# Optimization experiments

Measured on AMD Instinct MI355X. Metric: run time of the kernel, lower is better.

The kernel has to match this reference:

```python
import jax, jax.numpy as jnp
import numpy as np

LAG = 168
HORIZON = 24
D = 6            # d_model = 1 feature + 5-dim position embedding
FF = 18          # dim_feedforward
NL = 3           # num encoder layers
B = 8192
EPS = 1e-5


def setup_inputs() -> dict:
    key = jax.random.key(0)
    ks = jax.random.split(key, 16)
    s = 0.1
    return {
        "input": jax.random.normal(ks[0], (B, LAG), dtype=jnp.float32),
        "pos_emb": jax.random.normal(ks[1], (LAG, 5), dtype=jnp.float32) * s,
        "in_proj_w": jax.random.normal(ks[2], (NL, 3 * D, D), dtype=jnp.float32) * s,
        "in_proj_b": jax.random.normal(ks[3], (NL, 3 * D), dtype=jnp.float32) * s,
        "out_w": jax.random.normal(ks[4], (NL, D, D), dtype=jnp.float32) * s,
        "out_b": jax.random.normal(ks[5], (NL, D), dtype=jnp.float32) * s,
        "ln1_g": jnp.ones((NL, D), dtype=jnp.float32),
        "ln1_b": jnp.zeros((NL, D), dtype=jnp.float32),
        "lin1_w": jax.random.normal(ks[6], (NL, FF, D), dtype=jnp.float32) * s,
        "lin1_b": jax.random.normal(ks[7], (NL, FF), dtype=jnp.float32) * s,
        "lin2_w": jax.random.normal(ks[8], (NL, D, FF), dtype=jnp.float32) * s,
        "lin2_b": jax.random.normal(ks[9], (NL, D), dtype=jnp.float32) * s,
        "ln2_g": jnp.ones((NL, D), dtype=jnp.float32),
        "ln2_b": jnp.zeros((NL, D), dtype=jnp.float32),
        "head_w": jax.random.normal(ks[10], (HORIZON, D * LAG), dtype=jnp.float32) * s,
        "head_b": jax.random.normal(ks[11], (HORIZON,), dtype=jnp.float32) * s,
    }


def _layer_norm(x, g, b):
    m = jnp.mean(x, axis=-1, keepdims=True)
    v = jnp.mean((x - m) ** 2, axis=-1, keepdims=True)
    return (x - m) * jax.lax.rsqrt(v + EPS) * g + b


def reference(input, pos_emb, in_proj_w, in_proj_b, out_w, out_b,
              ln1_g, ln1_b, lin1_w, lin1_b, lin2_w, lin2_b,
              ln2_g, ln2_b, head_w, head_b):
    Bsz, L = input.shape
    # embed positions and concat with raw feature -> [B, L, 6]
    x = jnp.concatenate(
        [input[..., None], jnp.broadcast_to(pos_emb[None], (Bsz, L, 5))], axis=2)

    h = x
    scale = 1.0 / jnp.sqrt(jnp.float32(D))
    for i in range(NL):  # post-norm TransformerEncoderLayer (PyTorch default)
        qkv = jnp.einsum("bld,ed->ble", h, in_proj_w[i]) + in_proj_b[i]  # [B,L,18]
        q, k, v = jnp.split(qkv, 3, axis=-1)  # each [B,L,6], single head
        scores = jnp.einsum("bqd,bkd->bqk", q, k) * scale
        attn = jax.nn.softmax(scores, axis=-1)
        o = jnp.einsum("bqk,bkd->bqd", attn, v)
        o = jnp.einsum("bld,ed->ble", o, out_w[i]) + out_b[i]
        h = _layer_norm(h + o, ln1_g[i], ln1_b[i])
        f = jax.nn.relu(jnp.einsum("bld,fd->blf", h, lin1_w[i]) + lin1_b[i])
        f = jnp.einsum("blf,df->bld", f, lin2_w[i]) + lin2_b[i]
        h = _layer_norm(h + f, ln2_g[i], ln2_b[i])

    h = jax.nn.relu(h + x)              # residual from embedded input + relu
    h = h.reshape(Bsz, L * D)           # flatten
    return h @ head_w.T + head_b        # [B, HORIZON]
```

## Files before the change

### kernel.cpp

```cpp
#include <hip/hip_runtime.h>
#include <math.h>

#define LAG 168
#define HOR 24
#define DM 6
#define FFD 18
#define NL 3
#define WPB 4
#define LNEPS 1e-5f

typedef unsigned int u32;
typedef float f32x4 __attribute__((ext_vector_type(4)));
typedef float f32x16 __attribute__((ext_vector_type(16)));
typedef short s16x8 __attribute__((ext_vector_type(8)));
typedef __bf16 bfx2 __attribute__((ext_vector_type(2)));

#define PP    800
#define SLICE 1376

__device__ __forceinline__ u32 pkbf(float a, float b) {
    bfx2 t; t[0] = (__bf16)a; t[1] = (__bf16)b;
    return __builtin_bit_cast(u32, t);
}
__device__ __forceinline__ s16x8 mk8(u32 a, u32 b, u32 c, u32 d) {
    uint4 u; u.x = a; u.y = b; u.z = c; u.w = d;
    return __builtin_bit_cast(s16x8, u);
}
__device__ __forceinline__ float b2f(unsigned short h) {
    u32 u = ((u32)h) << 16; return __builtin_bit_cast(float, u);
}
__device__ __forceinline__ void ln6(const float* r, const float* g, const float* bb, float* outv) {
    float m = (r[0]+r[1]+r[2]+r[3]+r[4]+r[5]) * (1.0f/6.0f);
    float v = 0.f;
#pragma unroll
    for (int d = 0; d < DM; ++d) { float t = r[d]-m; v += t*t; }
    v *= (1.0f/6.0f);
    float rs = __builtin_amdgcn_rsqf(v + LNEPS);
#pragma unroll
    for (int d = 0; d < DM; ++d) outv[d] = (r[d]-m)*rs*g[d] + bb[d];
}

__global__ __launch_bounds__(64*WPB) void tfenc_kernel(
    const float* __restrict__ input, const float* __restrict__ pos_emb,
    const float* __restrict__ ipw, const float* __restrict__ ipb,
    const float* __restrict__ ow,  const float* __restrict__ obp,
    const float* __restrict__ l1g, const float* __restrict__ l1b,
    const float* __restrict__ f1w, const float* __restrict__ f1b,
    const float* __restrict__ f2w, const float* __restrict__ f2b,
    const float* __restrict__ l2g, const float* __restrict__ l2b,
    const float* __restrict__ hw,  const float* __restrict__ hb,
    float* __restrict__ out)
{
    __shared__ __align__(16) float lds[WPB * SLICE];

    const int L   = threadIdx.x & 63;
    const int wid = threadIdx.x >> 6;
    const int b   = blockIdx.x * WPB + wid;

    float*  sl  = lds + wid * SLICE;
    __bf16* slh = (__bf16*)sl;
    u32*    slu = (u32*)sl;

    float hv[3][DM], xv[3][DM];
#pragma unroll
    for (int i = 0; i < 3; ++i) {
        int r = L + 64*i;
        bool real = (r < LAG);
        xv[i][0] = real ? input[(size_t)b*LAG + r] : 0.f;
#pragma unroll
        for (int j = 0; j < 5; ++j)
            xv[i][1+j] = real ? pos_emb[r*5 + j] : 0.f;
#pragma unroll
        for (int d = 0; d < DM; ++d) hv[i][d] = xv[i][d];
    }

    const float cQ = 0.5889116917845058f;
    const u32 himask = (L & 32) ? 0u : ~0u;
    const int permA = 4*(L & 31);
    const int permB = permA + 128;

#pragma unroll 1
    for (int il = 0; il < NL; ++il) {
        const float* Wip = ipw + il*3*DM*DM;
        const float* bip = ipb + il*3*DM;
        const float* Wo  = ow  + il*DM*DM;
        const float* bo  = obp + il*DM;
        const float* g1  = l1g + il*DM;     const float* c1  = l1b + il*DM;
        const float* W1  = f1w + il*FFD*DM; const float* bb1 = f1b + il*FFD;
        const float* W2  = f2w + il*DM*FFD; const float* bb2 = f2b + il*DM;
        const float* g2  = l2g + il*DM;     const float* c2  = l2b + il*DM;

        u32 qp[3][3], kp[3][3];
#pragma unroll
        for (int i = 0; i < 3; ++i) {
            int r = L + 64*i;
            float qv[6], kv[6], vv[6];
#pragma unroll
            for (int e = 0; e < 18; ++e) {
                float a = bip[e];
#pragma unroll
                for (int d = 0; d < DM; ++d) a += hv[i][d]*Wip[e*DM+d];
                if (e < 6) qv[e] = a*cQ;
                else if (e < 12) kv[e-6] = a;
                else vv[e-12] = a;
            }
            qp[i][0]=pkbf(qv[0],qv[1]); qp[i][1]=pkbf(qv[2],qv[3]); qp[i][2]=pkbf(qv[4],qv[5]);
            kp[i][0]=pkbf(kv[0],kv[1]); kp[i][1]=pkbf(kv[2],kv[3]); kp[i][2]=pkbf(kv[4],kv[5]);
#pragma unroll
            for (int d = 0; d < DM; ++d)
                slh[d*200 + r] = (__bf16)vv[d];
        }
        {
            __bf16 one = (__bf16)1.0f;
            slh[6*200 + L] = one;
            slh[6*200 + 64 + L] = one;
            slh[6*200 + 128 + L] = one;
        }

        s16x8 kf[6];
#pragma unroll
        for (int kt = 0; kt < 6; ++kt) {
            int adr = (kt & 1) ? permB : permA;
            int slo = kt >> 1;
            u32 w0 = ((u32)__builtin_amdgcn_ds_bpermute(adr, (int)kp[slo][0])) & himask;
            u32 w1 = ((u32)__builtin_amdgcn_ds_bpermute(adr, (int)kp[slo][1])) & himask;
            u32 w2 = ((u32)__builtin_amdgcn_ds_bpermute(adr, (int)kp[slo][2])) & himask;
            kf[kt] = mk8(w0, w1, w2, 0u);
        }
        s16x8 vf[6];
        {
            int d = L & 15;
            int vrow = d < 7 ? d : 7;
            const u32* vb = slu + (vrow*100 + (L >> 4)*4);
#pragma unroll
            for (int kc = 0; kc < 6; ++kc)
                vf[kc] = __builtin_bit_cast(s16x8, *(const uint4*)(vb + kc*16));
        }

        const int wrbase = PP + (L & 31)*18 + 2*(L >> 5);
        const int rdbase = PP + (L & 15)*18 + 4*(L >> 4);

#pragma unroll
        for (int qt = 0; qt < 6; ++qt) {
            int adr = (qt & 1) ? permB : permA;
            int slo = qt >> 1;
            u32 u0 = ((u32)__builtin_amdgcn_ds_bpermute(adr, (int)qp[slo][0])) & himask;
            u32 u1 = ((u32)__builtin_amdgcn_ds_bpermute(adr, (int)qp[slo][1])) & himask;
            u32 u2 = ((u32)__builtin_amdgcn_ds_bpermute(adr, (int)qp[slo][2])) & himask;
            s16x8 qf = mk8(u0, u1, u2, 0u);
            f32x4 acc0 = {0.f,0.f,0.f,0.f};
            f32x4 acc1 = {0.f,0.f,0.f,0.f};
#pragma unroll
            for (int kt = 0; kt < 6; ++kt) {
                f32x16 z = {};
                f32x16 S = __builtin_amdgcn_mfma_f32_32x32x16_bf16(kf[kt], qf, z, 0, 0, 0);
                u32 w[8];
#pragma unroll
                for (int jj = 0; jj < 8; ++jj) {
                    float pa, pb;
                    if (kt == 5 && jj >= 2) { pa = 0.f; pb = 0.f; }
                    else {
                        pa = __builtin_amdgcn_exp2f(S[2*jj]);
                        pb = __builtin_amdgcn_exp2f(S[2*jj+1]);
                    }
                    w[jj] = pkbf(pa, pb);
                }
                u32* ppw = slu + wrbase;
                { uint2 t; t.x=w[0]; t.y=w[1]; *(uint2*)(ppw     ) = t; }
                { uint2 t; t.x=w[2]; t.y=w[3]; *(uint2*)(ppw +  4) = t; }
                { uint2 t; t.x=w[4]; t.y=w[5]; *(uint2*)(ppw +  8) = t; }
                { uint2 t; t.x=w[6]; t.y=w[7]; *(uint2*)(ppw + 12) = t; }
                const u32* rr = slu + rdbase;
                uint2 a00 = *(const uint2*)(rr);
                uint2 a01 = *(const uint2*)(rr + 2);
                uint2 a10 = *(const uint2*)(rr + 288);
                uint2 a11 = *(const uint2*)(rr + 290);
                acc0 = __builtin_amdgcn_mfma_f32_16x16x32_bf16(mk8(a00.x,a00.y,a01.x,a01.y), vf[kt], acc0, 0,0,0);
                acc1 = __builtin_amdgcn_mfma_f32_16x16x32_bf16(mk8(a10.x,a10.y,a11.x,a11.y), vf[kt], acc1, 0,0,0);
            }
            int d = L & 15;
            if (d < 7) {
                int qb = 32*qt + 4*(L >> 4);
#pragma unroll
                for (int r2 = 0; r2 < 4; ++r2) {
                    slh[(qb + r2)*8 + d]      = (__bf16)acc0[r2];
                    slh[(qb + 16 + r2)*8 + d] = (__bf16)acc1[r2];
                }
            }
        }

#pragma unroll
        for (int i = 0; i < 3; ++i) {
            int r = L + 64*i;
            s16x8 ov = __builtin_bit_cast(s16x8, *(const uint4*)(slh + r*8));
            float o[7];
#pragma unroll
            for (int d = 0; d < 7; ++d) o[d] = b2f((unsigned short)ov[d]);
            float inv = __builtin_amdgcn_rcpf(o[6]);
            float att[6], rv[6];
#pragma unroll
            for (int d = 0; d < 6; ++d) att[d] = o[d]*inv;
#pragma unroll
            for (int e = 0; e < 6; ++e) {
                float a = bo[e];
#pragma unroll
                for (int d = 0; d < 6; ++d) a += att[d]*Wo[e*6+d];
                rv[e] = hv[i][e] + a;
            }
            ln6(rv, g1, c1, hv[i]);
            float o2[6];
#pragma unroll
            for (int d = 0; d < 6; ++d) o2[d] = bb2[d];
#pragma unroll
            for (int ff = 0; ff < FFD; ++ff) {
                float a = bb1[ff];
#pragma unroll
                for (int d = 0; d < 6; ++d) a += hv[i][d]*W1[ff*6+d];
                a = fmaxf(a, 0.f);
#pragma unroll
                for (int d = 0; d < 6; ++d) o2[d] += a*W2[d*FFD+ff];
            }
#pragma unroll
            for (int d = 0; d < 6; ++d) rv[d] = hv[i][d] + o2[d];
            ln6(rv, g2, c2, hv[i]);
        }
    }

#pragma unroll
    for (int i = 0; i < 3; ++i) {
        int r = L + 64*i;
        bool real = (r < LAG);
#pragma unroll
        for (int d = 0; d < 6; ++d)
            sl[r*6 + d] = real ? fmaxf(hv[i][d] + xv[i][d], 0.f) : 0.f;
    }
    {
        int t = L >> 1, half = L & 1;
        float p = 0.f;
        if (L < 48) {
            const float4* wv  = (const float4*)(hw + (size_t)t*1008 + half*504);
            const float4* hv4 = (const float4*)(sl + half*504);
#pragma unroll 6
            for (int k = 0; k < 126; ++k) {
                float4 w = wv[k], h = hv4[k];
                p += w.x*h.x + w.y*h.y + w.z*h.z + w.w*h.w;
            }
        }
        p += __shfl_xor(p, 1);
        if (L < 48 && half == 0)
            out[(size_t)b*HOR + t] = p + hb[t];
    }
}

extern "C" void kernel_launch(void* const* d_in, const int* in_sizes, int n_in,
                              void* d_out, int out_size, void* d_ws, size_t ws_size,
                              hipStream_t stream) {
    const float* input   = (const float*)d_in[0];
    const float* pos_emb = (const float*)d_in[1];
    const float* ipw     = (const float*)d_in[2];
    const float* ipb     = (const float*)d_in[3];
    const float* ow      = (const float*)d_in[4];
    const float* ob      = (const float*)d_in[5];
    const float* l1g     = (const float*)d_in[6];
    const float* l1b     = (const float*)d_in[7];
    const float* f1w     = (const float*)d_in[8];
    const float* f1b     = (const float*)d_in[9];
    const float* f2w     = (const float*)d_in[10];
    const float* f2b     = (const float*)d_in[11];
    const float* l2g     = (const float*)d_in[12];
    const float* l2b     = (const float*)d_in[13];
    const float* hw      = (const float*)d_in[14];
    const float* hb      = (const float*)d_in[15];
    float* out = (float*)d_out;

    const int B = in_sizes[0] / LAG;
    tfenc_kernel<<<dim3(B / WPB), dim3(64 * WPB), 0, stream>>>(
        input, pos_emb, ipw, ipb, ow, ob, l1g, l1b,
        f1w, f1b, f2w, f2b, l2g, l2b, hw, hb, out);
}
```

Measured before the change: 186.0 us.

## Feed exp scores directly into 32x32 MFMA via permlane swap, drop LDS staging

The P·V product is restructured. Exponentiated score fragments are rearranged in registers with v_permlane32_swap and fed straight into a 32x32x16 MFMA that accumulates the output over all key tiles, with V read from LDS as the A operand. This removes the round trip of writing P to LDS and reading it back for two 16x16 MFMAs, and it drops the preloaded V fragments. The embedded input xv is no longer kept in registers and is reloaded from global memory at the end, which reduces register pressure at the cost of extra loads. The LDS slice grows to hold the new output area.

```diff
diff --git a/kernel.cpp b/kernel.cpp
--- a/kernel.cpp
+++ b/kernel.cpp
@@ -15,8 +15,8 @@
 typedef short s16x8 __attribute__((ext_vector_type(8)));
 typedef __bf16 bfx2 __attribute__((ext_vector_type(2)));
 
-#define PP    800
-#define SLICE 1376
+#define OOW   700
+#define SLICE 1472
 
 __device__ __forceinline__ u32 pkbf(float a, float b) {
     bfx2 t; t[0] = (__bf16)a; t[1] = (__bf16)b;
@@ -39,6 +39,8 @@
 #pragma unroll
     for (int d = 0; d < DM; ++d) outv[d] = (r[d]-m)*rs*g[d] + bb[d];
 }
+
+#define PSWAP(a, b) asm("v_permlane32_swap_b32 %0, %1" : "+v"(a), "+v"(b))
 
 __global__ __launch_bounds__(64*WPB) void tfenc_kernel(
     const float* __restrict__ input, const float* __restrict__ pos_emb,
@@ -61,23 +63,24 @@
     __bf16* slh = (__bf16*)sl;
     u32*    slu = (u32*)sl;
 
-    float hv[3][DM], xv[3][DM];
+    float hv[3][DM];
 #pragma unroll
     for (int i = 0; i < 3; ++i) {
         int r = L + 64*i;
         bool real = (r < LAG);
-        xv[i][0] = real ? input[(size_t)b*LAG + r] : 0.f;
+        hv[i][0] = real ? input[(size_t)b*LAG + r] : 0.f;
 #pragma unroll
         for (int j = 0; j < 5; ++j)
-            xv[i][1+j] = real ? pos_emb[r*5 + j] : 0.f;
-#pragma unroll
-        for (int d = 0; d < DM; ++d) hv[i][d] = xv[i][d];
+            hv[i][1+j] = real ? pos_emb[r*5 + j] : 0.f;
     }
 
     const float cQ = 0.5889116917845058f;
     const u32 himask = (L & 32) ? 0u : ~0u;
     const int permA = 4*(L & 31);
     const int permB = permA + 128;
+    const int h     = L >> 5;
+    const int vrow  = ((L & 31) < 7) ? (L & 31) : 6;
+    const int vbase = vrow*100 + 4*h;
 
 #pragma unroll 1
     for (int il = 0; il < NL; ++il) {
@@ -127,18 +130,6 @@
             u32 w2 = ((u32)__builtin_amdgcn_ds_bpermute(adr, (int)kp[slo][2])) & himask;
             kf[kt] = mk8(w0, w1, w2, 0u);
         }
-        s16x8 vf[6];
-        {
-            int d = L & 15;
-            int vrow = d < 7 ? d : 7;
-            const u32* vb = slu + (vrow*100 + (L >> 4)*4);
-#pragma unroll
-            for (int kc = 0; kc < 6; ++kc)
-                vf[kc] = __builtin_bit_cast(s16x8, *(const uint4*)(vb + kc*16));
-        }
-
-        const int wrbase = PP + (L & 31)*18 + 2*(L >> 5);
-        const int rdbase = PP + (L & 15)*18 + 4*(L >> 4);
 
 #pragma unroll
         for (int qt = 0; qt < 6; ++qt) {
@@ -148,51 +139,40 @@
             u32 u1 = ((u32)__builtin_amdgcn_ds_bpermute(adr, (int)qp[slo][1])) & himask;
             u32 u2 = ((u32)__builtin_amdgcn_ds_bpermute(adr, (int)qp[slo][2])) & himask;
             s16x8 qf = mk8(u0, u1, u2, 0u);
-            f32x4 acc0 = {0.f,0.f,0.f,0.f};
-            f32x4 acc1 = {0.f,0.f,0.f,0.f};
+            f32x16 osum = {};
 #pragma unroll
             for (int kt = 0; kt < 6; ++kt) {
-                f32x16 z = {};
+                const f32x16 z = {};
                 f32x16 S = __builtin_amdgcn_mfma_f32_32x32x16_bf16(kf[kt], qf, z, 0, 0, 0);
                 u32 w[8];
 #pragma unroll
                 for (int jj = 0; jj < 8; ++jj) {
-                    float pa, pb;
-                    if (kt == 5 && jj >= 2) { pa = 0.f; pb = 0.f; }
-                    else {
-                        pa = __builtin_amdgcn_exp2f(S[2*jj]);
-                        pb = __builtin_amdgcn_exp2f(S[2*jj+1]);
-                    }
-                    w[jj] = pkbf(pa, pb);
+                    if (kt == 5 && jj >= 2) w[jj] = 0u;
+                    else w[jj] = pkbf(__builtin_amdgcn_exp2f(S[2*jj]),
+                                      __builtin_amdgcn_exp2f(S[2*jj+1]));
                 }
-                u32* ppw = slu + wrbase;
-                { uint2 t; t.x=w[0]; t.y=w[1]; *(uint2*)(ppw     ) = t; }
-                { uint2 t; t.x=w[2]; t.y=w[3]; *(uint2*)(ppw +  4) = t; }
-                { uint2 t; t.x=w[4]; t.y=w[5]; *(uint2*)(ppw +  8) = t; }
-                { uint2 t; t.x=w[6]; t.y=w[7]; *(uint2*)(ppw + 12) = t; }
-                const u32* rr = slu + rdbase;
-                uint2 a00 = *(const uint2*)(rr);
-                uint2 a01 = *(const uint2*)(rr + 2);
-                uint2 a10 = *(const uint2*)(rr + 288);
-                uint2 a11 = *(const uint2*)(rr + 290);
-                acc0 = __builtin_amdgcn_mfma_f32_16x16x32_bf16(mk8(a00.x,a00.y,a01.x,a01.y), vf[kt], acc0, 0,0,0);
-                acc1 = __builtin_amdgcn_mfma_f32_16x16x32_bf16(mk8(a10.x,a10.y,a11.x,a11.y), vf[kt], acc1, 0,0,0);
-            }
-            int d = L & 15;
-            if (d < 7) {
-                int qb = 32*qt + 4*(L >> 4);
-#pragma unroll
-                for (int r2 = 0; r2 < 4; ++r2) {
-                    slh[(qb + r2)*8 + d]      = (__bf16)acc0[r2];
-                    slh[(qb + 16 + r2)*8 + d] = (__bf16)acc1[r2];
+                u32 s0 = w[0], s1 = w[1], s2 = w[2], s3 = w[3];
+                PSWAP(s0, s2); PSWAP(s1, s3);
+                const uint4* va = (const uint4*)(slu + vbase + 16*kt);
+                s16x8 A0 = __builtin_bit_cast(s16x8, va[0]);
+                osum = __builtin_amdgcn_mfma_f32_32x32x16_bf16(A0, mk8(s0,s1,s2,s3), osum, 0,0,0);
+                if (kt < 5) {
+                    u32 t0 = w[4], t1 = w[5], t2 = w[6], t3 = w[7];
+                    PSWAP(t0, t2); PSWAP(t1, t3);
+                    s16x8 A1 = __builtin_bit_cast(s16x8, va[2]);
+                    osum = __builtin_amdgcn_mfma_f32_32x32x16_bf16(A1, mk8(t0,t1,t2,t3), osum, 0,0,0);
                 }
             }
+            uint2 ot;
+            ot.x = pkbf(osum[0], osum[1]);
+            ot.y = pkbf(osum[2], osum[3]);
+            *(uint2*)(slu + OOW + (32*qt + (L & 31))*4 + 2*h) = ot;
         }
 
 #pragma unroll
         for (int i = 0; i < 3; ++i) {
             int r = L + 64*i;
-            s16x8 ov = __builtin_bit_cast(s16x8, *(const uint4*)(slh + r*8));
+            s16x8 ov = __builtin_bit_cast(s16x8, *(const uint4*)(slh + 2*OOW + r*8));
             float o[7];
 #pragma unroll
             for (int d = 0; d < 7; ++d) o[d] = b2f((unsigned short)ov[d]);
@@ -230,9 +210,13 @@
     for (int i = 0; i < 3; ++i) {
         int r = L + 64*i;
         bool real = (r < LAG);
-#pragma unroll
-        for (int d = 0; d < 6; ++d)
-            sl[r*6 + d] = real ? fmaxf(hv[i][d] + xv[i][d], 0.f) : 0.f;
+        float x0 = real ? input[(size_t)b*LAG + r] : 0.f;
+        sl[r*6 + 0] = real ? fmaxf(hv[i][0] + x0, 0.f) : 0.f;
+#pragma unroll
+        for (int j = 0; j < 5; ++j) {
+            float xj = real ? pos_emb[r*5 + j] : 0.f;
+            sl[r*6 + 1 + j] = real ? fmaxf(hv[i][1+j] + xj, 0.f) : 0.f;
+        }
     }
     {
         int t = L >> 1, half = L & 1;
@@ -242,8 +226,8 @@
             const float4* hv4 = (const float4*)(sl + half*504);
 #pragma unroll 6
             for (int k = 0; k < 126; ++k) {
-                float4 w = wv[k], h = hv4[k];
-                p += w.x*h.x + w.y*h.y + w.z*h.z + w.w*h.w;
+                float4 w = wv[k], hh = hv4[k];
+                p += w.x*hh.x + w.y*hh.y + w.z*hh.z + w.w*hh.w;
             }
         }
         p += __shfl_xor(p, 1);
```

Result: slower. 249.0 us (+33.9%).

## Cut register pressure, halve waves per block, add MFMA priority hints

Applied to the files above, without the earlier changes.

The kernel no longer keeps the embedded input (xv) in registers for all three layers. It reloads the input and position embedding from global memory at the final residual instead, which frees 18 VGPRs per thread for occupancy. Waves per block drop from 4 to 2, shrinking LDS per block so more blocks can be resident. s_setprio is raised around the MFMA instructions in the attention loop to favour matrix issue across waves. The cost is extra global reloads at the end and possibly worse scheduling if the priority hints misfire.

```diff
diff --git a/kernel.cpp b/kernel.cpp
--- a/kernel.cpp
+++ b/kernel.cpp
@@ -6,7 +6,7 @@
 #define DM 6
 #define FFD 18
 #define NL 3
-#define WPB 4
+#define WPB 2
 #define LNEPS 1e-5f
 
 typedef unsigned int u32;
@@ -61,17 +61,15 @@
     __bf16* slh = (__bf16*)sl;
     u32*    slu = (u32*)sl;
 
-    float hv[3][DM], xv[3][DM];
+    float hv[3][DM];
 #pragma unroll
     for (int i = 0; i < 3; ++i) {
         int r = L + 64*i;
         bool real = (r < LAG);
-        xv[i][0] = real ? input[(size_t)b*LAG + r] : 0.f;
+        hv[i][0] = real ? input[(size_t)b*LAG + r] : 0.f;
 #pragma unroll
         for (int j = 0; j < 5; ++j)
-            xv[i][1+j] = real ? pos_emb[r*5 + j] : 0.f;
-#pragma unroll
-        for (int d = 0; d < DM; ++d) hv[i][d] = xv[i][d];
+            hv[i][1+j] = real ? pos_emb[r*5 + j] : 0.f;
     }
 
     const float cQ = 0.5889116917845058f;
@@ -152,18 +150,16 @@
             f32x4 acc1 = {0.f,0.f,0.f,0.f};
 #pragma unroll
             for (int kt = 0; kt < 6; ++kt) {
-                f32x16 z = {};
+                const f32x16 z = {};
+                __builtin_amdgcn_s_setprio(1);
                 f32x16 S = __builtin_amdgcn_mfma_f32_32x32x16_bf16(kf[kt], qf, z, 0, 0, 0);
+                __builtin_amdgcn_s_setprio(0);
                 u32 w[8];
 #pragma unroll
                 for (int jj = 0; jj < 8; ++jj) {
-                    float pa, pb;
-                    if (kt == 5 && jj >= 2) { pa = 0.f; pb = 0.f; }
-                    else {
-                        pa = __builtin_amdgcn_exp2f(S[2*jj]);
-                        pb = __builtin_amdgcn_exp2f(S[2*jj+1]);
-                    }
-                    w[jj] = pkbf(pa, pb);
+                    if (kt == 5 && jj >= 2) w[jj] = 0u;
+                    else w[jj] = pkbf(__builtin_amdgcn_exp2f(S[2*jj]),
+                                      __builtin_amdgcn_exp2f(S[2*jj+1]));
                 }
                 u32* ppw = slu + wrbase;
                 { uint2 t; t.x=w[0]; t.y=w[1]; *(uint2*)(ppw     ) = t; }
@@ -175,8 +171,10 @@
                 uint2 a01 = *(const uint2*)(rr + 2);
                 uint2 a10 = *(const uint2*)(rr + 288);
                 uint2 a11 = *(const uint2*)(rr + 290);
+                __builtin_amdgcn_s_setprio(1);
                 acc0 = __builtin_amdgcn_mfma_f32_16x16x32_bf16(mk8(a00.x,a00.y,a01.x,a01.y), vf[kt], acc0, 0,0,0);
                 acc1 = __builtin_amdgcn_mfma_f32_16x16x32_bf16(mk8(a10.x,a10.y,a11.x,a11.y), vf[kt], acc1, 0,0,0);
+                __builtin_amdgcn_s_setprio(0);
             }
             int d = L & 15;
             if (d < 7) {
@@ -230,9 +228,13 @@
     for (int i = 0; i < 3; ++i) {
         int r = L + 64*i;
         bool real = (r < LAG);
-#pragma unroll
-        for (int d = 0; d < 6; ++d)
-            sl[r*6 + d] = real ? fmaxf(hv[i][d] + xv[i][d], 0.f) : 0.f;
+        float x0 = real ? input[(size_t)b*LAG + r] : 0.f;
+        sl[r*6 + 0] = real ? fmaxf(hv[i][0] + x0, 0.f) : 0.f;
+#pragma unroll
+        for (int j = 0; j < 5; ++j) {
+            float xj = real ? pos_emb[r*5 + j] : 0.f;
+            sl[r*6 + 1 + j] = real ? fmaxf(hv[i][1+j] + xj, 0.f) : 0.f;
+        }
     }
     {
         int t = L >> 1, half = L & 1;
@@ -242,8 +244,8 @@
             const float4* hv4 = (const float4*)(sl + half*504);
 #pragma unroll 6
             for (int k = 0; k < 126; ++k) {
-                float4 w = wv[k], h = hv4[k];
-                p += w.x*h.x + w.y*h.y + w.z*h.z + w.w*h.w;
+                float4 w = wv[k], hh = hv4[k];
+                p += w.x*hh.x + w.y*hh.y + w.z*hh.z + w.w*hh.w;
             }
         }
         p += __shfl_xor(p, 1);
```

Result: no change. 189.2 us (+1.7%).

## Distribute head projection across all lanes and shrink block to two waves

Applied to the files above, without the earlier changes.

The final head GEMV is restructured so that every lane multiplies its own three rows of activations against all 24 head outputs held in registers. Partial sums then go through LDS and are reduced by 24 lanes, replacing the old scheme where 48 lanes each streamed half of a 1008-length row. The block size drops from four waves to two, with a minimum-blocks launch bound and a larger per-wave LDS slice, which changes occupancy and register pressure. Small cleanups are included: a V row clamp index and a simpler zero-fill of masked softmax weights. The 24-element accumulator array raises register use, and the weight loads become strided float2 reads.

```diff
diff --git a/kernel.cpp b/kernel.cpp
--- a/kernel.cpp
+++ b/kernel.cpp
@@ -6,7 +6,7 @@
 #define DM 6
 #define FFD 18
 #define NL 3
-#define WPB 4
+#define WPB 2
 #define LNEPS 1e-5f
 
 typedef unsigned int u32;
@@ -16,7 +16,7 @@
 typedef __bf16 bfx2 __attribute__((ext_vector_type(2)));
 
 #define PP    800
-#define SLICE 1376
+#define SLICE 1600
 
 __device__ __forceinline__ u32 pkbf(float a, float b) {
     bfx2 t; t[0] = (__bf16)a; t[1] = (__bf16)b;
@@ -40,7 +40,7 @@
     for (int d = 0; d < DM; ++d) outv[d] = (r[d]-m)*rs*g[d] + bb[d];
 }
 
-__global__ __launch_bounds__(64*WPB) void tfenc_kernel(
+__global__ __launch_bounds__(64*WPB, 4) void tfenc_kernel(
     const float* __restrict__ input, const float* __restrict__ pos_emb,
     const float* __restrict__ ipw, const float* __restrict__ ipb,
     const float* __restrict__ ow,  const float* __restrict__ obp,
@@ -130,7 +130,7 @@
         s16x8 vf[6];
         {
             int d = L & 15;
-            int vrow = d < 7 ? d : 7;
+            int vrow = d < 7 ? d : 6;
             const u32* vb = slu + (vrow*100 + (L >> 4)*4);
 #pragma unroll
             for (int kc = 0; kc < 6; ++kc)
@@ -152,18 +152,14 @@
             f32x4 acc1 = {0.f,0.f,0.f,0.f};
 #pragma unroll
             for (int kt = 0; kt < 6; ++kt) {
-                f32x16 z = {};
+                const f32x16 z = {};
                 f32x16 S = __builtin_amdgcn_mfma_f32_32x32x16_bf16(kf[kt], qf, z, 0, 0, 0);
                 u32 w[8];
 #pragma unroll
                 for (int jj = 0; jj < 8; ++jj) {
-                    float pa, pb;
-                    if (kt == 5 && jj >= 2) { pa = 0.f; pb = 0.f; }
-                    else {
-                        pa = __builtin_amdgcn_exp2f(S[2*jj]);
-                        pb = __builtin_amdgcn_exp2f(S[2*jj+1]);
-                    }
-                    w[jj] = pkbf(pa, pb);
+                    if (kt == 5 && jj >= 2) w[jj] = 0u;
+                    else w[jj] = pkbf(__builtin_amdgcn_exp2f(S[2*jj]),
+                                      __builtin_amdgcn_exp2f(S[2*jj+1]));
                 }
                 u32* ppw = slu + wrbase;
                 { uint2 t; t.x=w[0]; t.y=w[1]; *(uint2*)(ppw     ) = t; }
@@ -226,29 +222,39 @@
         }
     }
 
+    float hf[3][6];
 #pragma unroll
     for (int i = 0; i < 3; ++i) {
         int r = L + 64*i;
         bool real = (r < LAG);
 #pragma unroll
         for (int d = 0; d < 6; ++d)
-            sl[r*6 + d] = real ? fmaxf(hv[i][d] + xv[i][d], 0.f) : 0.f;
-    }
-    {
-        int t = L >> 1, half = L & 1;
-        float p = 0.f;
-        if (L < 48) {
-            const float4* wv  = (const float4*)(hw + (size_t)t*1008 + half*504);
-            const float4* hv4 = (const float4*)(sl + half*504);
-#pragma unroll 6
-            for (int k = 0; k < 126; ++k) {
-                float4 w = wv[k], h = hv4[k];
-                p += w.x*h.x + w.y*h.y + w.z*h.z + w.w*h.w;
-            }
-        }
-        p += __shfl_xor(p, 1);
-        if (L < 48 && half == 0)
-            out[(size_t)b*HOR + t] = p + hb[t];
+            hf[i][d] = real ? fmaxf(hv[i][d] + xv[i][d], 0.f) : 0.f;
+    }
+    float pt[24];
+#pragma unroll
+    for (int t = 0; t < 24; ++t) pt[t] = 0.f;
+#pragma unroll
+    for (int i = 0; i < 3; ++i) {
+        int r = L + 64*i;
+        if (r < LAG) {
+            const float* wr = hw + r*6;
+#pragma unroll
+            for (int t = 0; t < 24; ++t) {
+                const float2* wp = (const float2*)(wr + t*1008);
+                float2 w0 = wp[0], w1 = wp[1], w2 = wp[2];
+                pt[t] += w0.x*hf[i][0] + w0.y*hf[i][1] + w1.x*hf[i][2]
+                       + w1.y*hf[i][3] + w2.x*hf[i][4] + w2.y*hf[i][5];
+            }
+        }
+    }
+#pragma unroll
+    for (int t = 0; t < 24; ++t) sl[L*25 + t] = pt[t];
+    if (L < HOR) {
+        float s = hb[L];
+#pragma unroll 8
+        for (int j = 0; j < 64; ++j) s += sl[j*25 + L];
+        out[(size_t)b*HOR + L] = s;
     }
 }
 
```

Result: slower. 249.7 us (+34.2%).
